# Optimization experiments

Hardware: AMD Instinct MI355X
Metric: run time of the kernel (lower is better)

Reference implementation:

```python
import jax, jax.numpy as jnp
import numpy as np

EMB = 768
HEADS = 12
DK = EMB // HEADS


def setup_inputs() -> dict:
    key = jax.random.key(0)
    ks = jax.random.split(key, 11)
    B, S = 2, 2048
    lim = 1.0 / np.sqrt(EMB)
    def lin(k):
        kw, kb = jax.random.split(k)
        W = jax.random.uniform(kw, (EMB, EMB), jnp.float32, -lim, lim)
        b = jax.random.uniform(kb, (EMB,), jnp.float32, -lim, lim)
        return W, b
    Wq, bq = lin(ks[0])
    Wk, bk = lin(ks[1])
    Wv, bv = lin(ks[2])
    Wo, bo = lin(ks[3])
    return {
        "query": jax.random.normal(ks[4], (B, S, EMB), jnp.float32),
        "key": jax.random.normal(ks[5], (B, S, EMB), jnp.float32),
        "value": jax.random.normal(ks[6], (B, S, EMB), jnp.float32),
        "Wq": Wq, "bq": bq, "Wk": Wk, "bk": bk,
        "Wv": Wv, "bv": bv, "Wo": Wo, "bo": bo,
    }


def reference(query, key, value, Wq, bq, Wk, bk, Wv, bv, Wo, bo):
    B, S, _ = query.shape
    # nn.Linear: x @ W^T + b, then split heads -> [B, H, S, d_k]
    def proj(x, W, b):
        return (x @ W.T + b).reshape(B, -1, HEADS, DK).transpose(0, 2, 1, 3)
    q = proj(query, Wq, bq)
    k = proj(key, Wk, bk)
    v = proj(value, Wv, bv)
    scale = 1.0 / jnp.sqrt(jnp.float32(DK))
    scores = jnp.einsum('bhqd,bhkd->bhqk', q, k) * scale  # [B,H,S,S]
    attn = jax.nn.softmax(scores, axis=-1)
    av = jnp.einsum('bhqk,bhkd->bhqd', attn, v)
    concat = av.transpose(0, 2, 1, 3).reshape(B, -1, EMB)
    return concat @ Wo.T + bo
```

## Files before the change

### kernel.cpp

```cpp
#include <hip/hip_runtime.h>
#include <hip/hip_bf16.h>

#define EMB 768
#define HEADS 12
#define DKV 64
#define BATCH 2
#define SEQ 2048
#define NTOK (BATCH*SEQ)

typedef float f32x4 __attribute__((ext_vector_type(4)));
typedef unsigned short u16;
typedef u16 u16x8 __attribute__((ext_vector_type(8)));
typedef u16 u16x4 __attribute__((ext_vector_type(4)));
typedef __bf16 bf16x8 __attribute__((ext_vector_type(8)));

__device__ __forceinline__ u16 f2bf(float f) {
  return __builtin_bit_cast(u16, (__bf16)f);
}
__device__ __forceinline__ float fexp2(float x) {
#if __has_builtin(__builtin_amdgcn_exp2f)
  return __builtin_amdgcn_exp2f(x);
#else
  return exp2f(x);
#endif
}
__device__ __forceinline__ f32x4 mfma16(u16x8 a, u16x8 b, f32x4 c) {
  return __builtin_amdgcn_mfma_f32_16x16x32_bf16(
      __builtin_bit_cast(bf16x8, a), __builtin_bit_cast(bf16x8, b), c, 0, 0, 0);
}
__device__ __forceinline__ void gload16(const void* g, void* l) {
  __builtin_amdgcn_global_load_lds(
      (const __attribute__((address_space(1))) void*)g,
      (__attribute__((address_space(3))) void*)l, 16, 0, 0);
}

__global__ void cast_all_k(
    const float* __restrict__ x0, const float* __restrict__ x1, const float* __restrict__ x2,
    const float* __restrict__ w0, const float* __restrict__ w1,
    const float* __restrict__ w2, const float* __restrict__ w3,
    u16* __restrict__ X0, u16* __restrict__ X1, u16* __restrict__ X2,
    u16* __restrict__ W0, u16* __restrict__ W1, u16* __restrict__ W2, u16* __restrict__ W3,
    float wscale0)
{
  const int NX = NTOK*EMB/8;
  const int NW = EMB*EMB/8;
  const int total = 3*NX + 4*NW;
  int i = blockIdx.x*256 + threadIdx.x;
  for (; i < total; i += gridDim.x*256) {
    const float* s; u16* d; int off; float sc = 1.f;
    if (i < 3*NX) {
      int which = i / NX; off = i - which*NX;
      s = which==0 ? x0 : which==1 ? x1 : x2;
      d = which==0 ? X0 : which==1 ? X1 : X2;
    } else {
      int j = i - 3*NX; int which = j / NW; off = j - which*NW;
      s = which==0 ? w0 : which==1 ? w1 : which==2 ? w2 : w3;
      d = which==0 ? W0 : which==1 ? W1 : which==2 ? W2 : W3;
      if (which == 0) sc = wscale0;
    }
    float4 a = reinterpret_cast<const float4*>(s)[off*2];
    float4 b = reinterpret_cast<const float4*>(s)[off*2+1];
    u16x8 o;
    o[0]=f2bf(a.x*sc); o[1]=f2bf(a.y*sc); o[2]=f2bf(a.z*sc); o[3]=f2bf(a.w*sc);
    o[4]=f2bf(b.x*sc); o[5]=f2bf(b.y*sc); o[6]=f2bf(b.z*sc); o[7]=f2bf(b.w*sc);
    reinterpret_cast<u16x8*>(d)[off] = o;
  }
}

template<int MODE>
__device__ __forceinline__ void gemm_core(
    const u16* __restrict__ A, const u16* __restrict__ Bm,
    const float* __restrict__ bias, float bscale, void* __restrict__ outp,
    u16* __restrict__ At, u16* __restrict__ Bt, int m0, int n0)
{
  const int t = threadIdx.x;
  const int w = t >> 6, lane = t & 63, lg = lane >> 4, lr = lane & 15;
  const int wr = w >> 1, wc = w & 1;

  f32x4 acc[4][4] = {};

  const int crow = (w*4)*8 + (lane >> 3);
  const int csl  = lane & 7;

  auto STAGE = [&](int kb) {
    #pragma unroll
    for (int i = 0; i < 4; ++i) {
      int row = crow + i*8;
      int sg = csl ^ (row & 7);
      gload16(A  + (size_t)(m0+row)*EMB + kb + sg*8, &At[(w*4+i)*512]);
      gload16(Bm + (size_t)(n0+row)*EMB + kb + sg*8, &Bt[(w*4+i)*512]);
    }
  };

  auto COMPUTE = [&]() {
    u16x8 af[4][2], bf[4][2];
    #pragma unroll
    for (int fm = 0; fm < 4; ++fm)
      #pragma unroll
      for (int kk = 0; kk < 2; ++kk) {
        int r = wr*64 + fm*16 + lr;
        int p = (lg + 4*kk) ^ (r & 7);
        af[fm][kk] = *reinterpret_cast<const u16x8*>(&At[r*64 + p*8]);
      }
    #pragma unroll
    for (int fn = 0; fn < 4; ++fn)
      #pragma unroll
      for (int kk = 0; kk < 2; ++kk) {
        int r = wc*64 + fn*16 + lr;
        int p = (lg + 4*kk) ^ (r & 7);
        bf[fn][kk] = *reinterpret_cast<const u16x8*>(&Bt[r*64 + p*8]);
      }
    __builtin_amdgcn_s_setprio(1);
    #pragma unroll
    for (int fm = 0; fm < 4; ++fm)
      #pragma unroll
      for (int fn = 0; fn < 4; ++fn)
        #pragma unroll
        for (int kk = 0; kk < 2; ++kk)
          acc[fm][fn] = mfma16(af[fm][kk], bf[fn][kk], acc[fm][fn]);
    __builtin_amdgcn_s_setprio(0);
  };

  const int NSTEP = EMB/64;
  #pragma unroll
  for (int ts = 0; ts < NSTEP; ++ts) {
    STAGE(ts*64);
    __syncthreads();
    COMPUTE();
    if (ts+1 < NSTEP) __syncthreads();
  }

  #pragma unroll
  for (int fm = 0; fm < 4; ++fm)
    #pragma unroll
    for (int fn = 0; fn < 4; ++fn) {
      const int mb = m0 + wr*64 + fm*16 + lg*4;
      const int e  = n0 + wc*64 + fn*16 + lr;
      if constexpr (MODE == 2) {
        int bb = mb >> 11, sb = mb & 2047, h = e >> 6, d = e & 63;
        u16x4 o4;
        #pragma unroll
        for (int j = 0; j < 4; ++j) o4[j] = f2bf(acc[fm][fn][j] + bias[e]*bscale);
        *reinterpret_cast<u16x4*>(
            reinterpret_cast<u16*>(outp) + (((size_t)(bb*HEADS+h))*DKV + d)*SEQ + sb) = o4;
      } else {
        #pragma unroll
        for (int j = 0; j < 4; ++j) {
          int m = mb + j;
          float val = acc[fm][fn][j] + bias[e]*bscale;
          if constexpr (MODE == 0) {
            int bb = m >> 11, s = m & 2047, h = e >> 6, d = e & 63;
            reinterpret_cast<u16*>(outp)[(((size_t)(bb*HEADS+h))*SEQ + s)*DKV + d] = f2bf(val);
          } else {
            reinterpret_cast<float*>(outp)[(size_t)m*EMB + e] = val;
          }
        }
      }
    }
}

__global__ __launch_bounds__(256) void qkv_k(
    const u16* __restrict__ Xq, const u16* __restrict__ Xk, const u16* __restrict__ Xv,
    const u16* __restrict__ Wq, const u16* __restrict__ Wk, const u16* __restrict__ Wv,
    const float* __restrict__ bq, const float* __restrict__ bk, const float* __restrict__ bv,
    u16* __restrict__ Qh, u16* __restrict__ Kh, u16* __restrict__ Vh, float csc)
{
  __shared__ __align__(16) u16 At[128*64];
  __shared__ __align__(16) u16 Bt[128*64];
  const int m0 = blockIdx.x*128, n0 = blockIdx.y*128;
  const int z = blockIdx.z;
  if (z == 0)
    gemm_core<0>(Xq, Wq, bq, csc, Qh, At, Bt, m0, n0);
  else if (z == 1)
    gemm_core<0>(Xk, Wk, bk, 1.f, Kh, At, Bt, m0, n0);
  else
    gemm_core<2>(Xv, Wv, bv, 1.f, Vh, At, Bt, m0, n0);
}

__global__ __launch_bounds__(256) void gemm_out_k(
    const u16* __restrict__ A, const u16* __restrict__ Bm,
    const float* __restrict__ bias, float* __restrict__ outp)
{
  __shared__ __align__(16) u16 At[128*64];
  __shared__ __align__(16) u16 Bt[128*64];
  gemm_core<1>(A, Bm, bias, 1.f, outp, At, Bt, blockIdx.x*128, blockIdx.y*128);
}

__global__ __launch_bounds__(256) void flash_attn_k(
    const u16* __restrict__ Q, const u16* __restrict__ K, const u16* __restrict__ VT,
    u16* __restrict__ av)
{
  __shared__ __align__(16) u16 Kt[2][64*64];
  __shared__ __align__(16) u16 Vt[2][64*64];
  __shared__ __align__(16) u16 Pt[4][2][16*64];

  const int t = threadIdx.x;
  const int w = t >> 6, lane = t & 63, lg = lane >> 4, lr = lane & 15;
  const int tr = t >> 3, tsl = t & 7;
  const int qb = blockIdx.x;
  const int bh = blockIdx.y;
  const u16* Qb = Q  + (size_t)bh*SEQ*DKV;
  const u16* Kb = K  + (size_t)bh*SEQ*DKV;
  const u16* Vb = VT + (size_t)bh*DKV*SEQ;

  const int qrow = qb*64 + w*16 + lr;
  u16x8 qf[2];
  qf[0] = *reinterpret_cast<const u16x8*>(Qb + (size_t)qrow*DKV + lg*8);
  qf[1] = *reinterpret_cast<const u16x8*>(Qb + (size_t)qrow*DKV + 32 + lg*8);

  f32x4 acc[4] = {};
  float mrun = -1e30f, lrun = 0.f;
  f32x4 s[4];

  u16x8 ks[2], vs[2];
  auto LOADKV = [&](int kt0) {
    #pragma unroll
    for (int q = 0; q < 2; ++q) {
      int row = q*32 + tr;
      ks[q] = *reinterpret_cast<const u16x8*>(Kb + (size_t)(kt0+row)*DKV + tsl*8);
    }
    #pragma unroll
    for (int q = 0; q < 2; ++q) {
      int d = q*32 + tr;
      vs[q] = *reinterpret_cast<const u16x8*>(Vb + (size_t)d*SEQ + kt0 + tsl*8);
    }
  };

  const int NT = SEQ/64;

#define WKV(bi)                                                               \
  do {                                                                        \
    _Pragma("unroll")                                                         \
    for (int q = 0; q < 2; ++q) {                                             \
      int row = q*32 + tr;                                                    \
      *reinterpret_cast<u16x8*>(&Kt[bi][row*64 + ((tsl ^ (row & 7))*8)]) = ks[q]; \
    }                                                                         \
    _Pragma("unroll")                                                         \
    for (int q = 0; q < 2; ++q) {                                             \
      int d = q*32 + tr;                                                      \
      *reinterpret_cast<u16x8*>(&Vt[bi][d*64 + ((tsl ^ (d & 7))*8)]) = vs[q]; \
    }                                                                         \
  } while (0)

#define QK_MFMA(bi)                                                           \
  do {                                                                        \
    _Pragma("unroll")                                                         \
    for (int fc = 0; fc < 4; ++fc) {                                          \
      f32x4 z = {};                                                           \
      _Pragma("unroll")                                                       \
      for (int kk = 0; kk < 2; ++kk) {                                        \
        int r = fc*16 + lr;                                                   \
        int slot = (lg + 4*kk) ^ (r & 7);                                     \
        u16x8 kf = *reinterpret_cast<const u16x8*>(&Kt[bi][r*64 + slot*8]);   \
        z = mfma16(kf, qf[kk], z);                                            \
      }                                                                       \
      s[fc] = z;                                                              \
    }                                                                         \
  } while (0)

#define PV_MFMA(bi)                                                           \
  do {                                                                        \
    const char* Pr = reinterpret_cast<const char*>(&Pt[w][bi][0]);            \
    _Pragma("unroll")                                                         \
    for (int kk = 0; kk < 2; ++kk) {                                          \
      u16x8 pf = *reinterpret_cast<const u16x8*>(                             \
          Pr + lr*128 + (((kk*8 + lg*2) ^ ((lr & 7) << 1))*8));               \
      _Pragma("unroll")                                                       \
      for (int fc = 0; fc < 4; ++fc) {                                        \
        int rv = fc*16 + lr;                                                  \
        int slotv = (lg + 4*kk) ^ (rv & 7);                                   \
        u16x8 vf = *reinterpret_cast<const u16x8*>(&Vt[bi][rv*64 + slotv*8]); \
        acc[fc] = mfma16(vf, pf, acc[fc]);                                    \
      }                                                                       \
    }                                                                         \
  } while (0)

#define SOFTMAX_PW(bi)                                                        \
  do {                                                                        \
    float a0 = fmaxf(fmaxf(s[0][0], s[0][1]), s[0][2]);                       \
    float a1 = fmaxf(fmaxf(s[0][3], s[1][0]), s[1][1]);                       \
    float a2 = fmaxf(fmaxf(s[1][2], s[1][3]), s[2][0]);                       \
    float a3 = fmaxf(fmaxf(s[2][1], s[2][2]), s[2][3]);                       \
    float a4 = fmaxf(fmaxf(s[3][0], s[3][1]), s[3][2]);                       \
    float pmax = fmaxf(fmaxf(fmaxf(a0, a1), a2),                              \
                       fmaxf(fmaxf(a3, a4), s[3][3]));                        \
    if (__any(pmax > mrun + 8.f)) {          \
      float pm = fmaxf(pmax, __shfl_xor(pmax, 16));                           \
      pm = fmaxf(pm, __shfl_xor(pm, 32));                                     \
      float mnew = fmaxf(mrun, pm);                                           \
      float corr = fexp2(mrun - mnew);                                        \
      mrun = mnew; lrun *= corr;                                              \
      _Pragma("unroll")                                                       \
      for (int fc = 0; fc < 4; ++fc)                                          \
        _Pragma("unroll")                                                     \
        for (int j = 0; j < 4; ++j)                                           \
          acc[fc][j] *= corr;                                                 \
    }                                                                         \
    float p[4][4], rsv[4];                                                    \
    _Pragma("unroll")                                                         \
    for (int fc = 0; fc < 4; ++fc) {                                          \
      _Pragma("unroll")                                                       \
      for (int j = 0; j < 4; ++j) p[fc][j] = fexp2(s[fc][j] - mrun);          \
      rsv[fc] = (p[fc][0] + p[fc][1]) + (p[fc][2] + p[fc][3]);                \
    }                                                                         \
    lrun += (rsv[0] + rsv[1]) + (rsv[2] + rsv[3]);                            \
    char* Pw_ = reinterpret_cast<char*>(&Pt[w][bi][0]);                       \
    _Pragma("unroll")                                                         \
    for (int fc = 0; fc < 4; ++fc) {                                          \
      u16x4 q4;                                                               \
      _Pragma("unroll")                                                       \
      for (int j = 0; j < 4; ++j) q4[j] = f2bf(p[fc][j]);                     \
      *reinterpret_cast<u16x4*>(                                              \
          Pw_ + lr*128 + (((fc*4 + lg) ^ ((lr & 7) << 1))*8)) = q4;           \
    }                                                                         \
  } while (0)

#define ITER(bi, kt)                                                          \
  do {                                                                        \
    __builtin_amdgcn_s_setprio(1);                                            \
    QK_MFMA(bi);                                                              \
    PV_MFMA(bi^1);                                                            \
    __builtin_amdgcn_s_setprio(0);                                            \
    SOFTMAX_PW(bi);                                                           \
    __syncthreads();                       \
    if ((kt)+1 < NT) WKV(bi^1);                  \
    __syncthreads();                                    \
    if ((kt)+2 < NT) LOADKV(((kt)+2)*64);                                     \
  } while (0)

  LOADKV(0);
  WKV(0);
  __syncthreads();
  LOADKV(64);
  QK_MFMA(0);
  SOFTMAX_PW(0);
  WKV(1);
  __syncthreads();
  LOADKV(128);

  for (int kt = 1; kt+1 < NT; kt += 2) {
    ITER(1, kt);
    ITER(0, kt+1);
  }
  ITER(1, NT-1);

  PV_MFMA(1);
  float lt = lrun;
  lt += __shfl_xor(lt, 16);
  lt += __shfl_xor(lt, 32);
  const float inv = 1.0f / lt;

  const int b = bh / HEADS, h = bh % HEADS;
  #pragma unroll
  for (int fc = 0; fc < 4; ++fc) {
    u16x4 o4;
    #pragma unroll
    for (int j = 0; j < 4; ++j) o4[j] = f2bf(acc[fc][j] * inv);
    *reinterpret_cast<u16x4*>(
        av + ((size_t)(b*SEQ + qrow))*EMB + h*64 + fc*16 + lg*4) = o4;
  }
#undef ITER
#undef SOFTMAX_PW
#undef PV_MFMA
#undef QK_MFMA
#undef WKV
}

extern "C" void kernel_launch(void* const* d_in, const int* in_sizes, int n_in,
                              void* d_out, int out_size, void* d_ws, size_t ws_size,
                              hipStream_t stream) {
  const float* xq_f = (const float*)d_in[0];
  const float* xk_f = (const float*)d_in[1];
  const float* xv_f = (const float*)d_in[2];
  const float* Wq = (const float*)d_in[3];
  const float* bq = (const float*)d_in[4];
  const float* Wk = (const float*)d_in[5];
  const float* bk = (const float*)d_in[6];
  const float* Wv = (const float*)d_in[7];
  const float* bv = (const float*)d_in[8];
  const float* Wo = (const float*)d_in[9];
  const float* bo = (const float*)d_in[10];

  const size_t NX = (size_t)NTOK*EMB;
  const size_t NW = (size_t)EMB*EMB;
  u16* Xc0 = (u16*)d_ws;
  u16* Xc1 = Xc0 + NX;
  u16* Xc2 = Xc1 + NX;
  u16* Wc0 = Xc2 + NX;
  u16* Wc1 = Wc0 + NW;
  u16* Wc2 = Wc1 + NW;
  u16* Wc3 = Wc2 + NW;
  u16* Qh  = Wc3 + NW;
  u16* Kh  = Qh + NX;
  u16* Vh  = Kh + NX;
  u16* Xb  = Xc0;

  const float csc = 0.125f * 1.4426950408889634f;

  cast_all_k<<<dim3(2048), dim3(256), 0, stream>>>(
      xq_f, xk_f, xv_f, Wq, Wk, Wv, Wo,
      Xc0, Xc1, Xc2, Wc0, Wc1, Wc2, Wc3, csc);

  qkv_k<<<dim3(NTOK/128, EMB/128, 3), dim3(256), 0, stream>>>(
      Xc0, Xc1, Xc2, Wc0, Wc1, Wc2, bq, bk, bv, Qh, Kh, Vh, csc);

  flash_attn_k<<<dim3(SEQ/64, BATCH*HEADS), dim3(256), 0, stream>>>(Qh, Kh, Vh, Xb);

  gemm_out_k<<<dim3(NTOK/128, EMB/128), dim3(256), 0, stream>>>(Xb, Wc3, bo, (float*)d_out);
}
```

Before: 104.8 us.

## Rework flash attention with 32x32 MFMA, split-key waves and direct LDS K loads

Rewrites the flash attention kernel to use 32x32x16 bf16 MFMA. Each pair of waves shares 32 query rows and splits each 64-key tile between the two waves. The probabilities stay in registers as the B operand, so the per-wave P round trip through LDS goes away. K tiles are loaded directly into LDS with global_load_lds, V is staged through registers with a swizzled split write, and one barrier per tile replaces two. The two key halves are merged at the end with a log-sum-exp combine through LDS, which adds epilogue work and raises accumulator register pressure.

After: 119.8 us. 14.3% more time.

```diff
diff --git a/kernel.cpp b/kernel.cpp
--- a/kernel.cpp
+++ b/kernel.cpp
@@ -9,6 +9,7 @@
 #define NTOK (BATCH*SEQ)
 
 typedef float f32x4 __attribute__((ext_vector_type(4)));
+typedef float f32x16 __attribute__((ext_vector_type(16)));
 typedef unsigned short u16;
 typedef u16 u16x8 __attribute__((ext_vector_type(8)));
 typedef u16 u16x4 __attribute__((ext_vector_type(4)));
@@ -26,6 +27,10 @@
 }
 __device__ __forceinline__ f32x4 mfma16(u16x8 a, u16x8 b, f32x4 c) {
   return __builtin_amdgcn_mfma_f32_16x16x32_bf16(
+      __builtin_bit_cast(bf16x8, a), __builtin_bit_cast(bf16x8, b), c, 0, 0, 0);
+}
+__device__ __forceinline__ f32x16 mfma32(u16x8 a, u16x8 b, f32x16 c) {
+  return __builtin_amdgcn_mfma_f32_32x32x16_bf16(
       __builtin_bit_cast(bf16x8, a), __builtin_bit_cast(bf16x8, b), c, 0, 0, 0);
 }
 __device__ __forceinline__ void gload16(const void* g, void* l) {
@@ -192,178 +197,166 @@
 {
   __shared__ __align__(16) u16 Kt[2][64*64];
   __shared__ __align__(16) u16 Vt[2][64*64];
-  __shared__ __align__(16) u16 Pt[4][2][16*64];
 
   const int t = threadIdx.x;
-  const int w = t >> 6, lane = t & 63, lg = lane >> 4, lr = lane & 15;
-  const int tr = t >> 3, tsl = t & 7;
-  const int qb = blockIdx.x;
-  const int bh = blockIdx.y;
+  const int w = t >> 6, lane = t & 63;
+  const int hi = lane >> 5, q32 = lane & 31;
+  const int qg = w >> 1, kh = w & 1;
+  const int qb = blockIdx.x, bh = blockIdx.y;
   const u16* Qb = Q  + (size_t)bh*SEQ*DKV;
   const u16* Kb = K  + (size_t)bh*SEQ*DKV;
   const u16* Vb = VT + (size_t)bh*DKV*SEQ;
 
-  const int qrow = qb*64 + w*16 + lr;
-  u16x8 qf[2];
-  qf[0] = *reinterpret_cast<const u16x8*>(Qb + (size_t)qrow*DKV + lg*8);
-  qf[1] = *reinterpret_cast<const u16x8*>(Qb + (size_t)qrow*DKV + 32 + lg*8);
-
-  f32x4 acc[4] = {};
+  const int qrow = qb*64 + qg*32 + q32;
+  u16x8 qf[4];
+  #pragma unroll
+  for (int ks = 0; ks < 4; ++ks)
+    qf[ks] = *reinterpret_cast<const u16x8*>(Qb + (size_t)qrow*DKV + ks*16 + hi*8);
+
+  f32x16 acc[2] = {};
   float mrun = -1e30f, lrun = 0.f;
-  f32x4 s[4];
-
-  u16x8 ks[2], vs[2];
-  auto LOADKV = [&](int kt0) {
-    #pragma unroll
-    for (int q = 0; q < 2; ++q) {
-      int row = q*32 + tr;
-      ks[q] = *reinterpret_cast<const u16x8*>(Kb + (size_t)(kt0+row)*DKV + tsl*8);
-    }
-    #pragma unroll
-    for (int q = 0; q < 2; ++q) {
-      int d = q*32 + tr;
-      vs[q] = *reinterpret_cast<const u16x8*>(Vb + (size_t)d*SEQ + kt0 + tsl*8);
+
+  u16x8 vr[2];
+  auto STAGE_K = [&](int kt0, int bi) {
+    #pragma unroll
+    for (int c = 0; c < 2; ++c) {
+      int ls = t + c*256;
+      int row = ls >> 3, sl = ls & 7;
+      int sg = sl ^ (row & 7);
+      gload16(Kb + (size_t)(kt0+row)*DKV + sg*8, &Kt[bi][ls*8]);
     }
   };
+  auto LOAD_V = [&](int kt0) {
+    #pragma unroll
+    for (int c = 0; c < 2; ++c) {
+      int gc = t + c*256;
+      int row = gc >> 3, a = gc & 7;
+      vr[c] = *reinterpret_cast<const u16x8*>(Vb + (size_t)row*SEQ + kt0 + a*8);
+    }
+  };
 
   const int NT = SEQ/64;
 
-#define WKV(bi)                                                               \
+#define WRITE_V(bi)                                                           \
   do {                                                                        \
     _Pragma("unroll")                                                         \
-    for (int q = 0; q < 2; ++q) {                                             \
-      int row = q*32 + tr;                                                    \
-      *reinterpret_cast<u16x8*>(&Kt[bi][row*64 + ((tsl ^ (row & 7))*8)]) = ks[q]; \
-    }                                                                         \
-    _Pragma("unroll")                                                         \
-    for (int q = 0; q < 2; ++q) {                                             \
-      int d = q*32 + tr;                                                      \
-      *reinterpret_cast<u16x8*>(&Vt[bi][d*64 + ((tsl ^ (d & 7))*8)]) = vs[q]; \
+    for (int c = 0; c < 2; ++c) {                                             \
+      int gc = t + c*256;                                                     \
+      int row = gc >> 3, a = gc & 7;                                          \
+      int p0 = (2*(a>>1))   ^ (row & 7);                                      \
+      int p1 = (2*(a>>1)+1) ^ (row & 7);                                      \
+      int sub = (a & 1)*4;                                                    \
+      u16x4 lo4 = { vr[c][0], vr[c][1], vr[c][2], vr[c][3] };                 \
+      u16x4 hi4 = { vr[c][4], vr[c][5], vr[c][6], vr[c][7] };                 \
+      *reinterpret_cast<u16x4*>(&Vt[bi][row*64 + p0*8 + sub]) = lo4;          \
+      *reinterpret_cast<u16x4*>(&Vt[bi][row*64 + p1*8 + sub]) = hi4;          \
     }                                                                         \
   } while (0)
 
-#define QK_MFMA(bi)                                                           \
+#define TILE(bi, kt)                                                          \
   do {                                                                        \
-    _Pragma("unroll")                                                         \
-    for (int fc = 0; fc < 4; ++fc) {                                          \
-      f32x4 z = {};                                                           \
+    if ((kt)+1 < NT) { STAGE_K(((kt)+1)*64, (bi)^1); LOAD_V(((kt)+1)*64); }   \
+    f32x16 s = {};                                                            \
+    {                                                                         \
+      const int key = kh*32 + q32;                                            \
+      const int kbase = key*64;                                               \
+      __builtin_amdgcn_s_setprio(1);                                          \
       _Pragma("unroll")                                                       \
-      for (int kk = 0; kk < 2; ++kk) {                                        \
-        int r = fc*16 + lr;                                                   \
-        int slot = (lg + 4*kk) ^ (r & 7);                                     \
-        u16x8 kf = *reinterpret_cast<const u16x8*>(&Kt[bi][r*64 + slot*8]);   \
-        z = mfma16(kf, qf[kk], z);                                            \
+      for (int ks = 0; ks < 4; ++ks) {                                        \
+        int ph = (2*ks + hi) ^ (key & 7);                                     \
+        u16x8 kf = *reinterpret_cast<const u16x8*>(&Kt[bi][kbase + ph*8]);    \
+        s = mfma32(kf, qf[ks], s);                                            \
       }                                                                       \
-      s[fc] = z;                                                              \
+      __builtin_amdgcn_s_setprio(0);                                          \
     }                                                                         \
-  } while (0)
-
-#define PV_MFMA(bi)                                                           \
-  do {                                                                        \
-    const char* Pr = reinterpret_cast<const char*>(&Pt[w][bi][0]);            \
-    _Pragma("unroll")                                                         \
-    for (int kk = 0; kk < 2; ++kk) {                                          \
-      u16x8 pf = *reinterpret_cast<const u16x8*>(                             \
-          Pr + lr*128 + (((kk*8 + lg*2) ^ ((lr & 7) << 1))*8));               \
-      _Pragma("unroll")                                                       \
-      for (int fc = 0; fc < 4; ++fc) {                                        \
-        int rv = fc*16 + lr;                                                  \
-        int slotv = (lg + 4*kk) ^ (rv & 7);                                   \
-        u16x8 vf = *reinterpret_cast<const u16x8*>(&Vt[bi][rv*64 + slotv*8]); \
-        acc[fc] = mfma16(vf, pf, acc[fc]);                                    \
-      }                                                                       \
-    }                                                                         \
-  } while (0)
-
-#define SOFTMAX_PW(bi)                                                        \
-  do {                                                                        \
-    float a0 = fmaxf(fmaxf(s[0][0], s[0][1]), s[0][2]);                       \
-    float a1 = fmaxf(fmaxf(s[0][3], s[1][0]), s[1][1]);                       \
-    float a2 = fmaxf(fmaxf(s[1][2], s[1][3]), s[2][0]);                       \
-    float a3 = fmaxf(fmaxf(s[2][1], s[2][2]), s[2][3]);                       \
-    float a4 = fmaxf(fmaxf(s[3][0], s[3][1]), s[3][2]);                       \
-    float pmax = fmaxf(fmaxf(fmaxf(a0, a1), a2),                              \
-                       fmaxf(fmaxf(a3, a4), s[3][3]));                        \
-    if (__any(pmax > mrun + 8.f)) {          \
-      float pm = fmaxf(pmax, __shfl_xor(pmax, 16));                           \
-      pm = fmaxf(pm, __shfl_xor(pm, 32));                                     \
+    float m0_ = fmaxf(fmaxf(s[0],s[1]), fmaxf(s[2],s[3]));                    \
+    float m1_ = fmaxf(fmaxf(s[4],s[5]), fmaxf(s[6],s[7]));                    \
+    float m2_ = fmaxf(fmaxf(s[8],s[9]), fmaxf(s[10],s[11]));                  \
+    float m3_ = fmaxf(fmaxf(s[12],s[13]), fmaxf(s[14],s[15]));                \
+    float pmax = fmaxf(fmaxf(m0_, m1_), fmaxf(m2_, m3_));                     \
+    if (__any(pmax > mrun + 8.f)) {                                           \
+      float pm = fmaxf(pmax, __shfl_xor(pmax, 32));                           \
       float mnew = fmaxf(mrun, pm);                                           \
       float corr = fexp2(mrun - mnew);                                        \
       mrun = mnew; lrun *= corr;                                              \
+      acc[0] = acc[0] * corr;                                                 \
+      acc[1] = acc[1] * corr;                                                 \
+    }                                                                         \
+    float p_[16];                                                             \
+    _Pragma("unroll")                                                         \
+    for (int r = 0; r < 16; ++r) p_[r] = fexp2(s[r] - mrun);                  \
+    lrun += ((p_[0]+p_[1])+(p_[2]+p_[3])) + ((p_[4]+p_[5])+(p_[6]+p_[7]))     \
+          + ((p_[8]+p_[9])+(p_[10]+p_[11])) + ((p_[12]+p_[13])+(p_[14]+p_[15])); \
+    u16x8 pa0, pa1;                                                           \
+    _Pragma("unroll")                                                         \
+    for (int j = 0; j < 8; ++j) { pa0[j] = f2bf(p_[j]); pa1[j] = f2bf(p_[8+j]); } \
+    {                                                                         \
+      __builtin_amdgcn_s_setprio(1);                                          \
       _Pragma("unroll")                                                       \
-      for (int fc = 0; fc < 4; ++fc)                                          \
-        _Pragma("unroll")                                                     \
-        for (int j = 0; j < 4; ++j)                                           \
-          acc[fc][j] *= corr;                                                 \
+      for (int ks = 0; ks < 2; ++ks) {                                        \
+        int ksg = kh*2 + ks;                                                  \
+        u16x8 pav = ks ? pa1 : pa0;                                           \
+        int ph = (2*ksg + hi) ^ (q32 & 7);                                    \
+        u16x8 v0 = *reinterpret_cast<const u16x8*>(&Vt[bi][q32*64 + ph*8]);   \
+        acc[0] = mfma32(v0, pav, acc[0]);                                     \
+        u16x8 v1 = *reinterpret_cast<const u16x8*>(&Vt[bi][(32+q32)*64 + ph*8]); \
+        acc[1] = mfma32(v1, pav, acc[1]);                                     \
+      }                                                                       \
+      __builtin_amdgcn_s_setprio(0);                                          \
     }                                                                         \
-    float p[4][4], rsv[4];                                                    \
-    _Pragma("unroll")                                                         \
-    for (int fc = 0; fc < 4; ++fc) {                                          \
-      _Pragma("unroll")                                                       \
-      for (int j = 0; j < 4; ++j) p[fc][j] = fexp2(s[fc][j] - mrun);          \
-      rsv[fc] = (p[fc][0] + p[fc][1]) + (p[fc][2] + p[fc][3]);                \
-    }                                                                         \
-    lrun += (rsv[0] + rsv[1]) + (rsv[2] + rsv[3]);                            \
-    char* Pw_ = reinterpret_cast<char*>(&Pt[w][bi][0]);                       \
-    _Pragma("unroll")                                                         \
-    for (int fc = 0; fc < 4; ++fc) {                                          \
-      u16x4 q4;                                                               \
-      _Pragma("unroll")                                                       \
-      for (int j = 0; j < 4; ++j) q4[j] = f2bf(p[fc][j]);                     \
-      *reinterpret_cast<u16x4*>(                                              \
-          Pw_ + lr*128 + (((fc*4 + lg) ^ ((lr & 7) << 1))*8)) = q4;           \
-    }                                                                         \
+    if ((kt)+1 < NT) WRITE_V((bi)^1);                                         \
+    __syncthreads();                                                          \
   } while (0)
 
-#define ITER(bi, kt)                                                          \
-  do {                                                                        \
-    __builtin_amdgcn_s_setprio(1);                                            \
-    QK_MFMA(bi);                                                              \
-    PV_MFMA(bi^1);                                                            \
-    __builtin_amdgcn_s_setprio(0);                                            \
-    SOFTMAX_PW(bi);                                                           \
-    __syncthreads();                       \
-    if ((kt)+1 < NT) WKV(bi^1);                  \
-    __syncthreads();                                    \
-    if ((kt)+2 < NT) LOADKV(((kt)+2)*64);                                     \
-  } while (0)
-
-  LOADKV(0);
-  WKV(0);
+  STAGE_K(0, 0); LOAD_V(0);
+  WRITE_V(0);
   __syncthreads();
-  LOADKV(64);
-  QK_MFMA(0);
-  SOFTMAX_PW(0);
-  WKV(1);
+
+  for (int kt = 0; kt < NT; kt += 2) {
+    TILE(0, kt);
+    TILE(1, kt+1);
+  }
+#undef TILE
+#undef WRITE_V
+
+  lrun += __shfl_xor(lrun, 32);
+  float* sc = reinterpret_cast<float*>(&Kt[0][0]);
+  float2* ml = reinterpret_cast<float2*>(&Vt[0][0]);
+
+  if (kh == 1) {
+    #pragma unroll
+    for (int db = 0; db < 2; ++db)
+      #pragma unroll
+      for (int g4 = 0; g4 < 4; ++g4) {
+        int ph = (db*4 + g4) ^ (lane & 7);
+        f32x4 v = { acc[db][g4*4+0], acc[db][g4*4+1], acc[db][g4*4+2], acc[db][g4*4+3] };
+        *reinterpret_cast<f32x4*>(&sc[qg*2048 + lane*32 + ph*4]) = v;
+      }
+    float2 m2; m2.x = mrun; m2.y = lrun;
+    ml[qg*64 + lane] = m2;
+  }
   __syncthreads();
-  LOADKV(128);
-
-  for (int kt = 1; kt+1 < NT; kt += 2) {
-    ITER(1, kt);
-    ITER(0, kt+1);
+  if (kh == 0) {
+    float2 mo = ml[qg*64 + lane];
+    float g  = fmaxf(mrun, mo.x);
+    float wsf = fexp2(mrun - g), wof = fexp2(mo.x - g);
+    float inv = 1.0f / (lrun*wsf + mo.y*wof);
+    wsf *= inv; wof *= inv;
+    const int b = bh / HEADS, h = bh % HEADS;
+    u16* op = av + ((size_t)(b*SEQ + qrow))*EMB + h*64;
+    #pragma unroll
+    for (int db = 0; db < 2; ++db)
+      #pragma unroll
+      for (int rg = 0; rg < 4; ++rg) {
+        int ph = (db*4 + rg) ^ (lane & 7);
+        f32x4 o = *reinterpret_cast<const f32x4*>(&sc[qg*2048 + lane*32 + ph*4]);
+        u16x4 o4;
+        #pragma unroll
+        for (int c = 0; c < 4; ++c)
+          o4[c] = f2bf(acc[db][rg*4+c]*wsf + o[c]*wof);
+        *reinterpret_cast<u16x4*>(op + db*32 + rg*8 + hi*4) = o4;
+      }
   }
-  ITER(1, NT-1);
-
-  PV_MFMA(1);
-  float lt = lrun;
-  lt += __shfl_xor(lt, 16);
-  lt += __shfl_xor(lt, 32);
-  const float inv = 1.0f / lt;
-
-  const int b = bh / HEADS, h = bh % HEADS;
-  #pragma unroll
-  for (int fc = 0; fc < 4; ++fc) {
-    u16x4 o4;
-    #pragma unroll
-    for (int j = 0; j < 4; ++j) o4[j] = f2bf(acc[fc][j] * inv);
-    *reinterpret_cast<u16x4*>(
-        av + ((size_t)(b*SEQ + qrow))*EMB + h*64 + fc*16 + lg*4) = o4;
-  }
-#undef ITER
-#undef SOFTMAX_PW
-#undef PV_MFMA
-#undef QK_MFMA
-#undef WKV
 }
 
 extern "C" void kernel_launch(void* const* d_in, const int* in_sizes, int n_in,
```

## Load K/V fragments directly from global in flash attention, remap grid for L2

Applied to the files above, without the earlier changes.

Removes the shared-memory staging and double buffering of K and V tiles in the attention kernel. Each wave now reads its MFMA operand fragments straight from global memory and relies on the cache, which drops the two block-wide barriers per tile and most of the LDS footprint. The grid is flattened to 1D and remapped so that 8 consecutive blocks cover 8 different heads at the same query block, which is meant to help K/V cache locality across workgroups. The cost is redundant global loads across the four waves and loss of software prefetch overlap, so load latency may be exposed.

Measured after the change: 230.6 us. 2.2x slower.

```diff
diff --git a/kernel.cpp b/kernel.cpp
--- a/kernel.cpp
+++ b/kernel.cpp
@@ -190,15 +190,13 @@
     const u16* __restrict__ Q, const u16* __restrict__ K, const u16* __restrict__ VT,
     u16* __restrict__ av)
 {
-  __shared__ __align__(16) u16 Kt[2][64*64];
-  __shared__ __align__(16) u16 Vt[2][64*64];
-  __shared__ __align__(16) u16 Pt[4][2][16*64];
+  __shared__ __align__(16) u16 Pt[4][16*64];
 
   const int t = threadIdx.x;
   const int w = t >> 6, lane = t & 63, lg = lane >> 4, lr = lane & 15;
-  const int tr = t >> 3, tsl = t & 7;
-  const int qb = blockIdx.x;
-  const int bh = blockIdx.y;
+  const int id = blockIdx.x;
+  const int bh = (id & 7) + 8*(id >> 8);
+  const int qb = (id >> 3) & 31;
   const u16* Qb = Q  + (size_t)bh*SEQ*DKV;
   const u16* Kb = K  + (size_t)bh*SEQ*DKV;
   const u16* Vb = VT + (size_t)bh*DKV*SEQ;
@@ -208,143 +206,83 @@
   qf[0] = *reinterpret_cast<const u16x8*>(Qb + (size_t)qrow*DKV + lg*8);
   qf[1] = *reinterpret_cast<const u16x8*>(Qb + (size_t)qrow*DKV + 32 + lg*8);
 
+  const u16* kbase = Kb + (size_t)lr*DKV + lg*8;
+  const u16* vbase = Vb + (size_t)lr*SEQ + lg*8;
+
   f32x4 acc[4] = {};
   float mrun = -1e30f, lrun = 0.f;
-  f32x4 s[4];
-
-  u16x8 ks[2], vs[2];
-  auto LOADKV = [&](int kt0) {
-    #pragma unroll
-    for (int q = 0; q < 2; ++q) {
-      int row = q*32 + tr;
-      ks[q] = *reinterpret_cast<const u16x8*>(Kb + (size_t)(kt0+row)*DKV + tsl*8);
-    }
-    #pragma unroll
-    for (int q = 0; q < 2; ++q) {
-      int d = q*32 + tr;
-      vs[q] = *reinterpret_cast<const u16x8*>(Vb + (size_t)d*SEQ + kt0 + tsl*8);
-    }
-  };
-
-  const int NT = SEQ/64;
-
-#define WKV(bi)                                                               \
-  do {                                                                        \
-    _Pragma("unroll")                                                         \
-    for (int q = 0; q < 2; ++q) {                                             \
-      int row = q*32 + tr;                                                    \
-      *reinterpret_cast<u16x8*>(&Kt[bi][row*64 + ((tsl ^ (row & 7))*8)]) = ks[q]; \
-    }                                                                         \
-    _Pragma("unroll")                                                         \
-    for (int q = 0; q < 2; ++q) {                                             \
-      int d = q*32 + tr;                                                      \
-      *reinterpret_cast<u16x8*>(&Vt[bi][d*64 + ((tsl ^ (d & 7))*8)]) = vs[q]; \
-    }                                                                         \
-  } while (0)
-
-#define QK_MFMA(bi)                                                           \
-  do {                                                                        \
-    _Pragma("unroll")                                                         \
-    for (int fc = 0; fc < 4; ++fc) {                                          \
-      f32x4 z = {};                                                           \
-      _Pragma("unroll")                                                       \
-      for (int kk = 0; kk < 2; ++kk) {                                        \
-        int r = fc*16 + lr;                                                   \
-        int slot = (lg + 4*kk) ^ (r & 7);                                     \
-        u16x8 kf = *reinterpret_cast<const u16x8*>(&Kt[bi][r*64 + slot*8]);   \
-        z = mfma16(kf, qf[kk], z);                                            \
-      }                                                                       \
-      s[fc] = z;                                                              \
-    }                                                                         \
-  } while (0)
-
-#define PV_MFMA(bi)                                                           \
-  do {                                                                        \
-    const char* Pr = reinterpret_cast<const char*>(&Pt[w][bi][0]);            \
-    _Pragma("unroll")                                                         \
-    for (int kk = 0; kk < 2; ++kk) {                                          \
-      u16x8 pf = *reinterpret_cast<const u16x8*>(                             \
-          Pr + lr*128 + (((kk*8 + lg*2) ^ ((lr & 7) << 1))*8));               \
-      _Pragma("unroll")                                                       \
-      for (int fc = 0; fc < 4; ++fc) {                                        \
-        int rv = fc*16 + lr;                                                  \
-        int slotv = (lg + 4*kk) ^ (rv & 7);                                   \
-        u16x8 vf = *reinterpret_cast<const u16x8*>(&Vt[bi][rv*64 + slotv*8]); \
-        acc[fc] = mfma16(vf, pf, acc[fc]);                                    \
-      }                                                                       \
-    }                                                                         \
-  } while (0)
-
-#define SOFTMAX_PW(bi)                                                        \
-  do {                                                                        \
-    float a0 = fmaxf(fmaxf(s[0][0], s[0][1]), s[0][2]);                       \
-    float a1 = fmaxf(fmaxf(s[0][3], s[1][0]), s[1][1]);                       \
-    float a2 = fmaxf(fmaxf(s[1][2], s[1][3]), s[2][0]);                       \
-    float a3 = fmaxf(fmaxf(s[2][1], s[2][2]), s[2][3]);                       \
-    float a4 = fmaxf(fmaxf(s[3][0], s[3][1]), s[3][2]);                       \
-    float pmax = fmaxf(fmaxf(fmaxf(a0, a1), a2),                              \
-                       fmaxf(fmaxf(a3, a4), s[3][3]));                        \
-    if (__any(pmax > mrun + 8.f)) {          \
-      float pm = fmaxf(pmax, __shfl_xor(pmax, 16));                           \
-      pm = fmaxf(pm, __shfl_xor(pm, 32));                                     \
-      float mnew = fmaxf(mrun, pm);                                           \
-      float corr = fexp2(mrun - mnew);                                        \
-      mrun = mnew; lrun *= corr;                                              \
-      _Pragma("unroll")                                                       \
-      for (int fc = 0; fc < 4; ++fc)                                          \
-        _Pragma("unroll")                                                     \
-        for (int j = 0; j < 4; ++j)                                           \
-          acc[fc][j] *= corr;                                                 \
-    }                                                                         \
-    float p[4][4], rsv[4];                                                    \
-    _Pragma("unroll")                                                         \
-    for (int fc = 0; fc < 4; ++fc) {                                          \
-      _Pragma("unroll")                                                       \
-      for (int j = 0; j < 4; ++j) p[fc][j] = fexp2(s[fc][j] - mrun);          \
-      rsv[fc] = (p[fc][0] + p[fc][1]) + (p[fc][2] + p[fc][3]);                \
-    }                                                                         \
-    lrun += (rsv[0] + rsv[1]) + (rsv[2] + rsv[3]);                            \
-    char* Pw_ = reinterpret_cast<char*>(&Pt[w][bi][0]);                       \
-    _Pragma("unroll")                                                         \
-    for (int fc = 0; fc < 4; ++fc) {                                          \
-      u16x4 q4;                                                               \
-      _Pragma("unroll")                                                       \
-      for (int j = 0; j < 4; ++j) q4[j] = f2bf(p[fc][j]);                     \
-      *reinterpret_cast<u16x4*>(                                              \
-          Pw_ + lr*128 + (((fc*4 + lg) ^ ((lr & 7) << 1))*8)) = q4;           \
-    }                                                                         \
-  } while (0)
-
-#define ITER(bi, kt)                                                          \
-  do {                                                                        \
-    __builtin_amdgcn_s_setprio(1);                                            \
-    QK_MFMA(bi);                                                              \
-    PV_MFMA(bi^1);                                                            \
-    __builtin_amdgcn_s_setprio(0);                                            \
-    SOFTMAX_PW(bi);                                                           \
-    __syncthreads();                       \
-    if ((kt)+1 < NT) WKV(bi^1);                  \
-    __syncthreads();                                    \
-    if ((kt)+2 < NT) LOADKV(((kt)+2)*64);                                     \
-  } while (0)
-
-  LOADKV(0);
-  WKV(0);
-  __syncthreads();
-  LOADKV(64);
-  QK_MFMA(0);
-  SOFTMAX_PW(0);
-  WKV(1);
-  __syncthreads();
-  LOADKV(128);
-
-  for (int kt = 1; kt+1 < NT; kt += 2) {
-    ITER(1, kt);
-    ITER(0, kt+1);
+  char* Pw = reinterpret_cast<char*>(&Pt[w][0]);
+
+  for (int kt0 = 0; kt0 < SEQ; kt0 += 64) {
+    f32x4 s[4];
+    __builtin_amdgcn_s_setprio(1);
+    #pragma unroll
+    for (int fc = 0; fc < 4; ++fc) {
+      f32x4 z = {};
+      #pragma unroll
+      for (int kk = 0; kk < 2; ++kk) {
+        u16x8 kf = *reinterpret_cast<const u16x8*>(
+            kbase + (size_t)(kt0 + fc*16)*DKV + kk*32);
+        z = mfma16(kf, qf[kk], z);
+      }
+      s[fc] = z;
+    }
+    __builtin_amdgcn_s_setprio(0);
+
+    float a0 = fmaxf(fmaxf(s[0][0], s[0][1]), s[0][2]);
+    float a1 = fmaxf(fmaxf(s[0][3], s[1][0]), s[1][1]);
+    float a2 = fmaxf(fmaxf(s[1][2], s[1][3]), s[2][0]);
+    float a3 = fmaxf(fmaxf(s[2][1], s[2][2]), s[2][3]);
+    float a4 = fmaxf(fmaxf(s[3][0], s[3][1]), s[3][2]);
+    float pmax = fmaxf(fmaxf(fmaxf(a0, a1), a2),
+                       fmaxf(fmaxf(a3, a4), s[3][3]));
+    if (__any(pmax > mrun + 8.f)) {
+      float pm = fmaxf(pmax, __shfl_xor(pmax, 16));
+      pm = fmaxf(pm, __shfl_xor(pm, 32));
+      float mnew = fmaxf(mrun, pm);
+      float corr = fexp2(mrun - mnew);
+      mrun = mnew; lrun *= corr;
+      #pragma unroll
+      for (int fc = 0; fc < 4; ++fc)
+        #pragma unroll
+        for (int j = 0; j < 4; ++j)
+          acc[fc][j] *= corr;
+    }
+    float p[4][4], rsv[4];
+    #pragma unroll
+    for (int fc = 0; fc < 4; ++fc) {
+      #pragma unroll
+      for (int j = 0; j < 4; ++j) p[fc][j] = fexp2(s[fc][j] - mrun);
+      rsv[fc] = (p[fc][0] + p[fc][1]) + (p[fc][2] + p[fc][3]);
+    }
+    lrun += (rsv[0] + rsv[1]) + (rsv[2] + rsv[3]);
+
+    #pragma unroll
+    for (int fc = 0; fc < 4; ++fc) {
+      u16x4 q4;
+      #pragma unroll
+      for (int j = 0; j < 4; ++j) q4[j] = f2bf(p[fc][j]);
+      *reinterpret_cast<u16x4*>(
+          Pw + lr*128 + (((fc*4 + lg) ^ ((lr & 7) << 1))*8)) = q4;
+    }
+    asm volatile("s_waitcnt lgkmcnt(0)" ::: "memory");
+    __builtin_amdgcn_sched_barrier(0);
+
+    __builtin_amdgcn_s_setprio(1);
+    #pragma unroll
+    for (int kk = 0; kk < 2; ++kk) {
+      u16x8 pf = *reinterpret_cast<const u16x8*>(
+          Pw + lr*128 + (((kk*8 + lg*2) ^ ((lr & 7) << 1))*8));
+      #pragma unroll
+      for (int fc = 0; fc < 4; ++fc) {
+        u16x8 vf = *reinterpret_cast<const u16x8*>(
+            vbase + (size_t)(fc*16)*SEQ + kt0 + kk*32);
+        acc[fc] = mfma16(vf, pf, acc[fc]);
+      }
+    }
+    __builtin_amdgcn_s_setprio(0);
   }
-  ITER(1, NT-1);
-
-  PV_MFMA(1);
+
   float lt = lrun;
   lt += __shfl_xor(lt, 16);
   lt += __shfl_xor(lt, 32);
@@ -359,11 +297,6 @@
     *reinterpret_cast<u16x4*>(
         av + ((size_t)(b*SEQ + qrow))*EMB + h*64 + fc*16 + lg*4) = o4;
   }
-#undef ITER
-#undef SOFTMAX_PW
-#undef PV_MFMA
-#undef QK_MFMA
-#undef WKV
 }
 
 extern "C" void kernel_launch(void* const* d_in, const int* in_sizes, int n_in,
@@ -404,7 +337,7 @@
   qkv_k<<<dim3(NTOK/128, EMB/128, 3), dim3(256), 0, stream>>>(
       Xc0, Xc1, Xc2, Wc0, Wc1, Wc2, bq, bk, bv, Qh, Kh, Vh, csc);
 
-  flash_attn_k<<<dim3(SEQ/64, BATCH*HEADS), dim3(256), 0, stream>>>(Qh, Kh, Vh, Xb);
+  flash_attn_k<<<dim3(SEQ/64 * BATCH*HEADS), dim3(256), 0, stream>>>(Qh, Kh, Vh, Xb);
 
   gemm_out_k<<<dim3(NTOK/128, EMB/128), dim3(256), 0, stream>>>(Xb, Wc3, bo, (float*)d_out);
 }
```

## Halve GEMM M-tile and restructure flash attention into single-tile loop

Applied to the files above, without the earlier changes.

The projection and output GEMMs move from 128x128 to 64x128 tiles, doubling block count to fill more CUs (out GEMM had only 192 blocks). The flash attention kernel drops the software-pipelined schedule that overlapped QK of tile i with PV of tile i-1 via double-buffered P. It now does QK, softmax and PV for the same tile in sequence, with one barrier per tile instead of two and K/V prefetch issued at the start of the tile. This trades cross-tile MFMA overlap for fewer barriers and less P shared memory, and smaller GEMM tiles lower per-block data reuse.

New measurement: 96.39 us. 1.09x faster.

```diff
diff --git a/kernel.cpp b/kernel.cpp
--- a/kernel.cpp
+++ b/kernel.cpp
@@ -77,28 +77,35 @@
   const int w = t >> 6, lane = t & 63, lg = lane >> 4, lr = lane & 15;
   const int wr = w >> 1, wc = w & 1;
 
-  f32x4 acc[4][4] = {};
-
-  const int crow = (w*4)*8 + (lane >> 3);
+  f32x4 acc[2][4] = {};
+
+  const int lrow = lane >> 3;
   const int csl  = lane & 7;
 
   auto STAGE = [&](int kb) {
     #pragma unroll
+    for (int i = 0; i < 2; ++i) {
+      int ci = w*2 + i;
+      int row = ci*8 + lrow;
+      int sg = csl ^ (row & 7);
+      gload16(A + (size_t)(m0+row)*EMB + kb + sg*8, &At[ci*512]);
+    }
+    #pragma unroll
     for (int i = 0; i < 4; ++i) {
-      int row = crow + i*8;
+      int ci = w*4 + i;
+      int row = ci*8 + lrow;
       int sg = csl ^ (row & 7);
-      gload16(A  + (size_t)(m0+row)*EMB + kb + sg*8, &At[(w*4+i)*512]);
-      gload16(Bm + (size_t)(n0+row)*EMB + kb + sg*8, &Bt[(w*4+i)*512]);
+      gload16(Bm + (size_t)(n0+row)*EMB + kb + sg*8, &Bt[ci*512]);
     }
   };
 
   auto COMPUTE = [&]() {
-    u16x8 af[4][2], bf[4][2];
-    #pragma unroll
-    for (int fm = 0; fm < 4; ++fm)
+    u16x8 af[2][2], bf[4][2];
+    #pragma unroll
+    for (int fm = 0; fm < 2; ++fm)
       #pragma unroll
       for (int kk = 0; kk < 2; ++kk) {
-        int r = wr*64 + fm*16 + lr;
+        int r = wr*32 + fm*16 + lr;
         int p = (lg + 4*kk) ^ (r & 7);
         af[fm][kk] = *reinterpret_cast<const u16x8*>(&At[r*64 + p*8]);
       }
@@ -112,7 +119,7 @@
       }
     __builtin_amdgcn_s_setprio(1);
     #pragma unroll
-    for (int fm = 0; fm < 4; ++fm)
+    for (int fm = 0; fm < 2; ++fm)
       #pragma unroll
       for (int fn = 0; fn < 4; ++fn)
         #pragma unroll
@@ -131,10 +138,10 @@
   }
 
   #pragma unroll
-  for (int fm = 0; fm < 4; ++fm)
+  for (int fm = 0; fm < 2; ++fm)
     #pragma unroll
     for (int fn = 0; fn < 4; ++fn) {
-      const int mb = m0 + wr*64 + fm*16 + lg*4;
+      const int mb = m0 + wr*32 + fm*16 + lg*4;
       const int e  = n0 + wc*64 + fn*16 + lr;
       if constexpr (MODE == 2) {
         int bb = mb >> 11, sb = mb & 2047, h = e >> 6, d = e & 63;
@@ -165,9 +172,9 @@
     const float* __restrict__ bq, const float* __restrict__ bk, const float* __restrict__ bv,
     u16* __restrict__ Qh, u16* __restrict__ Kh, u16* __restrict__ Vh, float csc)
 {
-  __shared__ __align__(16) u16 At[128*64];
+  __shared__ __align__(16) u16 At[64*64];
   __shared__ __align__(16) u16 Bt[128*64];
-  const int m0 = blockIdx.x*128, n0 = blockIdx.y*128;
+  const int m0 = blockIdx.x*64, n0 = blockIdx.y*128;
   const int z = blockIdx.z;
   if (z == 0)
     gemm_core<0>(Xq, Wq, bq, csc, Qh, At, Bt, m0, n0);
@@ -181,9 +188,9 @@
     const u16* __restrict__ A, const u16* __restrict__ Bm,
     const float* __restrict__ bias, float* __restrict__ outp)
 {
-  __shared__ __align__(16) u16 At[128*64];
+  __shared__ __align__(16) u16 At[64*64];
   __shared__ __align__(16) u16 Bt[128*64];
-  gemm_core<1>(A, Bm, bias, 1.f, outp, At, Bt, blockIdx.x*128, blockIdx.y*128);
+  gemm_core<1>(A, Bm, bias, 1.f, outp, At, Bt, blockIdx.x*64, blockIdx.y*128);
 }
 
 __global__ __launch_bounds__(256) void flash_attn_k(
@@ -192,7 +199,7 @@
 {
   __shared__ __align__(16) u16 Kt[2][64*64];
   __shared__ __align__(16) u16 Vt[2][64*64];
-  __shared__ __align__(16) u16 Pt[4][2][16*64];
+  __shared__ __align__(16) u16 Pt[4][16*64];
 
   const int t = threadIdx.x;
   const int w = t >> 6, lane = t & 63, lg = lane >> 4, lr = lane & 15;
@@ -210,7 +217,6 @@
 
   f32x4 acc[4] = {};
   float mrun = -1e30f, lrun = 0.f;
-  f32x4 s[4];
 
   u16x8 ks[2], vs[2];
   auto LOADKV = [&](int kt0) {
@@ -227,23 +233,28 @@
   };
 
   const int NT = SEQ/64;
-
-#define WKV(bi)                                                               \
+  LOADKV(0);
+  {
+    #pragma unroll
+    for (int q = 0; q < 2; ++q) {
+      int row = q*32 + tr;
+      *reinterpret_cast<u16x8*>(&Kt[0][row*64 + ((tsl ^ (row & 7))*8)]) = ks[q];
+    }
+    #pragma unroll
+    for (int q = 0; q < 2; ++q) {
+      int d = q*32 + tr;
+      *reinterpret_cast<u16x8*>(&Vt[0][d*64 + ((tsl ^ (d & 7))*8)]) = vs[q];
+    }
+  }
+  __syncthreads();
+
+  char* Pw = reinterpret_cast<char*>(&Pt[w][0]);
+
+#define TILE(bi, kt)                                                          \
   do {                                                                        \
-    _Pragma("unroll")                                                         \
-    for (int q = 0; q < 2; ++q) {                                             \
-      int row = q*32 + tr;                                                    \
-      *reinterpret_cast<u16x8*>(&Kt[bi][row*64 + ((tsl ^ (row & 7))*8)]) = ks[q]; \
-    }                                                                         \
-    _Pragma("unroll")                                                         \
-    for (int q = 0; q < 2; ++q) {                                             \
-      int d = q*32 + tr;                                                      \
-      *reinterpret_cast<u16x8*>(&Vt[bi][d*64 + ((tsl ^ (d & 7))*8)]) = vs[q]; \
-    }                                                                         \
-  } while (0)
-
-#define QK_MFMA(bi)                                                           \
-  do {                                                                        \
+    if ((kt)+1 < NT) LOADKV(((kt)+1)*64);                                     \
+    f32x4 s[4];                                                               \
+    __builtin_amdgcn_s_setprio(1);                                            \
     _Pragma("unroll")                                                         \
     for (int fc = 0; fc < 4; ++fc) {                                          \
       f32x4 z = {};                                                           \
@@ -256,27 +267,7 @@
       }                                                                       \
       s[fc] = z;                                                              \
     }                                                                         \
-  } while (0)
-
-#define PV_MFMA(bi)                                                           \
-  do {                                                                        \
-    const char* Pr = reinterpret_cast<const char*>(&Pt[w][bi][0]);            \
-    _Pragma("unroll")                                                         \
-    for (int kk = 0; kk < 2; ++kk) {                                          \
-      u16x8 pf = *reinterpret_cast<const u16x8*>(                             \
-          Pr + lr*128 + (((kk*8 + lg*2) ^ ((lr & 7) << 1))*8));               \
-      _Pragma("unroll")                                                       \
-      for (int fc = 0; fc < 4; ++fc) {                                        \
-        int rv = fc*16 + lr;                                                  \
-        int slotv = (lg + 4*kk) ^ (rv & 7);                                   \
-        u16x8 vf = *reinterpret_cast<const u16x8*>(&Vt[bi][rv*64 + slotv*8]); \
-        acc[fc] = mfma16(vf, pf, acc[fc]);                                    \
-      }                                                                       \
-    }                                                                         \
-  } while (0)
-
-#define SOFTMAX_PW(bi)                                                        \
-  do {                                                                        \
+    __builtin_amdgcn_s_setprio(0);                                            \
     float a0 = fmaxf(fmaxf(s[0][0], s[0][1]), s[0][2]);                       \
     float a1 = fmaxf(fmaxf(s[0][3], s[1][0]), s[1][1]);                       \
     float a2 = fmaxf(fmaxf(s[1][2], s[1][3]), s[2][0]);                       \
@@ -296,55 +287,61 @@
         for (int j = 0; j < 4; ++j)                                           \
           acc[fc][j] *= corr;                                                 \
     }                                                                         \
-    float p[4][4], rsv[4];                                                    \
+    float p[4][4], rs[4];                                                     \
     _Pragma("unroll")                                                         \
     for (int fc = 0; fc < 4; ++fc) {                                          \
       _Pragma("unroll")                                                       \
       for (int j = 0; j < 4; ++j) p[fc][j] = fexp2(s[fc][j] - mrun);          \
-      rsv[fc] = (p[fc][0] + p[fc][1]) + (p[fc][2] + p[fc][3]);                \
-    }                                                                         \
-    lrun += (rsv[0] + rsv[1]) + (rsv[2] + rsv[3]);                            \
-    char* Pw_ = reinterpret_cast<char*>(&Pt[w][bi][0]);                       \
+      rs[fc] = (p[fc][0] + p[fc][1]) + (p[fc][2] + p[fc][3]);                 \
+    }                                                                         \
+    lrun += (rs[0] + rs[1]) + (rs[2] + rs[3]);      \
     _Pragma("unroll")                                                         \
     for (int fc = 0; fc < 4; ++fc) {                                          \
       u16x4 q4;                                                               \
       _Pragma("unroll")                                                       \
       for (int j = 0; j < 4; ++j) q4[j] = f2bf(p[fc][j]);                     \
       *reinterpret_cast<u16x4*>(                                              \
-          Pw_ + lr*128 + (((fc*4 + lg) ^ ((lr & 7) << 1))*8)) = q4;           \
-    }                                                                         \
+          Pw + lr*128 + (((fc*4 + lg) ^ ((lr & 7) << 1))*8)) = q4;            \
+    }                                                                         \
+    asm volatile("s_waitcnt lgkmcnt(0)" ::: "memory");                        \
+    __builtin_amdgcn_sched_barrier(0);                                        \
+    __builtin_amdgcn_s_setprio(1);                                            \
+    _Pragma("unroll")                                                         \
+    for (int kk = 0; kk < 2; ++kk) {                                          \
+      u16x8 pf = *reinterpret_cast<const u16x8*>(                             \
+          Pw + lr*128 + (((kk*8 + lg*2) ^ ((lr & 7) << 1))*8));               \
+      _Pragma("unroll")                                                       \
+      for (int fc = 0; fc < 4; ++fc) {                                        \
+        int rv = fc*16 + lr;                                                  \
+        int slotv = (lg + 4*kk) ^ (rv & 7);                                   \
+        u16x8 vf = *reinterpret_cast<const u16x8*>(&Vt[bi][rv*64 + slotv*8]); \
+        acc[fc] = mfma16(vf, pf, acc[fc]);                                    \
+      }                                                                       \
+    }                                                                         \
+    __builtin_amdgcn_s_setprio(0);                                            \
+    if ((kt)+1 < NT) {                                                        \
+      _Pragma("unroll")                                                       \
+      for (int q = 0; q < 2; ++q) {                                           \
+        int row = q*32 + tr;                                                  \
+        *reinterpret_cast<u16x8*>(                                            \
+            &Kt[(bi)^1][row*64 + ((tsl ^ (row & 7))*8)]) = ks[q];             \
+      }                                                                       \
+      _Pragma("unroll")                                                       \
+      for (int q = 0; q < 2; ++q) {                                           \
+        int d = q*32 + tr;                                                    \
+        *reinterpret_cast<u16x8*>(                                            \
+            &Vt[(bi)^1][d*64 + ((tsl ^ (d & 7))*8)]) = vs[q];                 \
+      }                                                                       \
+    }                                                                         \
+    __syncthreads();                                                          \
   } while (0)
 
-#define ITER(bi, kt)                                                          \
-  do {                                                                        \
-    __builtin_amdgcn_s_setprio(1);                                            \
-    QK_MFMA(bi);                                                              \
-    PV_MFMA(bi^1);                                                            \
-    __builtin_amdgcn_s_setprio(0);                                            \
-    SOFTMAX_PW(bi);                                                           \
-    __syncthreads();                       \
-    if ((kt)+1 < NT) WKV(bi^1);                  \
-    __syncthreads();                                    \
-    if ((kt)+2 < NT) LOADKV(((kt)+2)*64);                                     \
-  } while (0)
-
-  LOADKV(0);
-  WKV(0);
-  __syncthreads();
-  LOADKV(64);
-  QK_MFMA(0);
-  SOFTMAX_PW(0);
-  WKV(1);
-  __syncthreads();
-  LOADKV(128);
-
-  for (int kt = 1; kt+1 < NT; kt += 2) {
-    ITER(1, kt);
-    ITER(0, kt+1);
+  for (int kt = 0; kt < NT; kt += 2) {
+    TILE(0, kt);
+    TILE(1, kt+1);
   }
-  ITER(1, NT-1);
-
-  PV_MFMA(1);
+#undef TILE
+
   float lt = lrun;
   lt += __shfl_xor(lt, 16);
   lt += __shfl_xor(lt, 32);
@@ -359,11 +356,6 @@
     *reinterpret_cast<u16x4*>(
         av + ((size_t)(b*SEQ + qrow))*EMB + h*64 + fc*16 + lg*4) = o4;
   }
-#undef ITER
-#undef SOFTMAX_PW
-#undef PV_MFMA
-#undef QK_MFMA
-#undef WKV
 }
 
 extern "C" void kernel_launch(void* const* d_in, const int* in_sizes, int n_in,
@@ -401,10 +393,10 @@
       xq_f, xk_f, xv_f, Wq, Wk, Wv, Wo,
       Xc0, Xc1, Xc2, Wc0, Wc1, Wc2, Wc3, csc);
 
-  qkv_k<<<dim3(NTOK/128, EMB/128, 3), dim3(256), 0, stream>>>(
+  qkv_k<<<dim3(NTOK/64, EMB/128, 3), dim3(256), 0, stream>>>(
       Xc0, Xc1, Xc2, Wc0, Wc1, Wc2, bq, bk, bv, Qh, Kh, Vh, csc);
 
   flash_attn_k<<<dim3(SEQ/64, BATCH*HEADS), dim3(256), 0, stream>>>(Qh, Kh, Vh, Xb);
 
-  gemm_out_k<<<dim3(NTOK/128, EMB/128), dim3(256), 0, stream>>>(Xb, Wc3, bo, (float*)d_out);
-}
+  gemm_out_k<<<dim3(NTOK/64, EMB/128), dim3(256), 0, stream>>>(Xb, Wc3, bo, (float*)d_out);
+}
```
